# Performance work log

Measured on AMD Instinct MI355X. Metric: run time of the kernel, lower is better.

The kernel has to match this reference:

```python
import jax, jax.numpy as jnp
import numpy as np

EPS = 1e-5

def setup_inputs() -> dict:
    key = jax.random.key(0)
    k1, k2, k3, k4, k5 = jax.random.split(key, 5)
    B, D, S = 4096, 2048, 16384
    return {
        "x": jax.random.normal(k1, (B, D), dtype=jnp.float32),
        "W_enc": jax.random.normal(k2, (S, D), dtype=jnp.float32) * 0.02,  # encoder.weight [n_sae, n_input]
        "W_dec": jax.random.normal(k3, (D, S), dtype=jnp.float32) * 0.02,  # decoder.weight [n_input, n_sae]
        "pre_bias": jax.random.normal(k4, (D,), dtype=jnp.float32) * 0.01,
        "sae_bias": jax.random.normal(k5, (S,), dtype=jnp.float32) * 0.01,
        "k": 64,
    }

def reference(x, W_enc, W_dec, pre_bias, sae_bias, k):
    # --- pre_process: layer norm (torch.std is unbiased -> ddof=1) ---
    x_mean = jnp.mean(x, axis=-1, keepdims=True)
    std = jnp.std(x, axis=-1, ddof=1, keepdims=True)
    x_ln = (x - x_mean) / (std + EPS)
    # --- encode: latents_pre = (x_ln - pre_bias) @ W_enc^T + sae_bias ---
    pre_activations = (x_ln - pre_bias) @ W_enc.T + sae_bias  # [B, n_sae]
    # --- TopK activation: keep top-k, ReLU them, zero the rest ---
    vals, idx = jax.lax.top_k(pre_activations, k)              # [B, k]
    vals = jax.nn.relu(vals)
    rows = jnp.arange(pre_activations.shape[0])[:, None]       # [B, 1]
    latents = jnp.zeros_like(pre_activations).at[rows, idx].set(vals)
    # --- decode + un-normalize ---
    recons = latents @ W_dec.T + pre_bias                      # [B, n_input]
    recons = recons * std + x_mean
    return pre_activations, latents, recons
```

## Files before the change

kernel.cpp:

```cpp
#include <hip/hip_runtime.h>
#include <cstdint>
#include <cstddef>

#define EPSV 1e-5f
#define CAP 224
#define PAD 16
#define DELTA 0.02f
#define AMBCAP 64

__device__ __forceinline__ unsigned short f2bf(float f) {
  unsigned u = __float_as_uint(f);
  unsigned r = (u + 0x7FFFu + ((u >> 16) & 1u)) >> 16;
  return (unsigned short)r;
}
__device__ __forceinline__ float bf2f(unsigned short h) {
  return __uint_as_float(((unsigned)h) << 16);
}

__global__ __launch_bounds__(256) void ln_kernel(const float* __restrict__ x,
    const float* __restrict__ pre_bias, float* __restrict__ a,
    unsigned short* __restrict__ A2,
    float* __restrict__ stats, int D) {
  const int b = blockIdx.x;
  const int tid = threadIdx.x;
  const float4* x4 = reinterpret_cast<const float4*>(x + (size_t)b * D);
  const float4* pb4 = reinterpret_cast<const float4*>(pre_bias);
  float4* a4 = reinterpret_cast<float4*>(a + (size_t)b * D);
  float4 v0 = x4[tid], v1 = x4[tid + 256];
  float s = v0.x + v0.y + v0.z + v0.w + v1.x + v1.y + v1.z + v1.w;
  float ss = v0.x*v0.x + v0.y*v0.y + v0.z*v0.z + v0.w*v0.w
           + v1.x*v1.x + v1.y*v1.y + v1.z*v1.z + v1.w*v1.w;
#pragma unroll
  for (int off = 1; off < 64; off <<= 1) { s += __shfl_xor(s, off); ss += __shfl_xor(ss, off); }
  __shared__ float wsum[4], wssq[4], bmean, bstd;
  int wave = tid >> 6;
  if ((tid & 63) == 0) { wsum[wave] = s; wssq[wave] = ss; }
  __syncthreads();
  if (tid == 0) {
    float S1 = wsum[0] + wsum[1] + wsum[2] + wsum[3];
    float S2 = wssq[0] + wssq[1] + wssq[2] + wssq[3];
    float mean = S1 / (float)D;
    float var = (S2 - (float)D * mean * mean) / (float)(D - 1);
    float sd = sqrtf(fmaxf(var, 0.f));
    bmean = mean; bstd = sd;
    stats[2*b] = mean; stats[2*b+1] = sd;
  }
  __syncthreads();
  float mean = bmean, rstd = 1.f / (bstd + EPSV);
  float4 p0 = pb4[tid], p1 = pb4[tid + 256];
  float4 o0, o1;
  o0.x = (v0.x - mean) * rstd - p0.x; o0.y = (v0.y - mean) * rstd - p0.y;
  o0.z = (v0.z - mean) * rstd - p0.z; o0.w = (v0.w - mean) * rstd - p0.w;
  o1.x = (v1.x - mean) * rstd - p1.x; o1.y = (v1.y - mean) * rstd - p1.y;
  o1.z = (v1.z - mean) * rstd - p1.z; o1.w = (v1.w - mean) * rstd - p1.w;
  a4[tid] = o0; a4[tid + 256] = o1;
  if (A2) {
    unsigned short* row = A2 + (size_t)b * 2048;
    ushort4 h0 = make_ushort4(f2bf(o0.x), f2bf(o0.y), f2bf(o0.z), f2bf(o0.w));
    ushort4 h1 = make_ushort4(f2bf(o1.x), f2bf(o1.y), f2bf(o1.z), f2bf(o1.w));
    *reinterpret_cast<ushort4*>(row + tid * 4) = h0;
    *reinterpret_cast<ushort4*>(row + 1024 + tid * 4) = h1;
  }
}

__global__ __launch_bounds__(256) void cvt_w_kernel(const float* __restrict__ W,
    unsigned short* __restrict__ W2, int D) {
  const int s = blockIdx.x, tid = threadIdx.x;
  const float4* w4 = reinterpret_cast<const float4*>(W + (size_t)s * D);
  unsigned short* row = W2 + (size_t)s * D;
  float4 v0 = w4[tid * 2], v1 = w4[tid * 2 + 1];
  uint4 p;
  p.x = (unsigned)f2bf(v0.x) | ((unsigned)f2bf(v0.y) << 16);
  p.y = (unsigned)f2bf(v0.z) | ((unsigned)f2bf(v0.w) << 16);
  p.z = (unsigned)f2bf(v1.x) | ((unsigned)f2bf(v1.y) << 16);
  p.w = (unsigned)f2bf(v1.z) | ((unsigned)f2bf(v1.w) << 16);
  *reinterpret_cast<uint4*>(row + tid * 8) = p;
}

typedef __attribute__((ext_vector_type(8))) short bf8;
typedef __attribute__((ext_vector_type(4))) float f32x4;

__device__ __forceinline__ void gload16(const void* g, void* l) {
  __builtin_amdgcn_global_load_lds(
      (const __attribute__((address_space(1))) unsigned int*)g,
      (__attribute__((address_space(3))) unsigned int*)l,
      16, 0, 0);
}

__global__ __launch_bounds__(256) void enc_gemm_bf16(
    const unsigned short* __restrict__ A2,
    const unsigned short* __restrict__ W2,
    const float* __restrict__ sae_bias,
    float* __restrict__ C, int M, int N) {
  __shared__ __align__(16) short As0[128 * 64];
  __shared__ __align__(16) short Bs0[128 * 64];
  __shared__ __align__(16) short As1[128 * 64];
  __shared__ __align__(16) short Bs1[128 * 64];
  const int tid = threadIdx.x;
  const int bn = blockIdx.x, bm = blockIdx.y;
  const int w = tid >> 6, l = tid & 63;

  const int lrow = l >> 3;
  const int lcol = ((l & 7) ^ lrow) * 8;
  const unsigned short* gA[4];
  const unsigned short* gB[4];
#pragma unroll
  for (int i = 0; i < 4; ++i) {
    int chunk = w * 4 + i;
    int row = chunk * 8 + lrow;
    gA[i] = A2 + (size_t)(bm * 128 + row) * 2048 + lcol;
    gB[i] = W2 + (size_t)(bn * 128 + row) * 2048 + lcol;
  }
  const int ldsOff = (w * 4) * 512 + l * 8;

  const int wm = (w >> 1) * 64, wn = (w & 1) * 64;
  const int r15 = l & 15, b7 = l & 7, u = l >> 4;
  const int colks0 = ((u + 0) ^ b7) * 8;
  const int colks1 = ((u + 4) ^ b7) * 8;
  const int baseA = (wm + r15) * 64;
  const int baseB = (wn + r15) * 64;

  f32x4 acc[4][4];
#pragma unroll
  for (int mi = 0; mi < 4; ++mi)
#pragma unroll
    for (int ni = 0; ni < 4; ++ni) acc[mi][ni] = (f32x4){0.f, 0.f, 0.f, 0.f};

#define STAGE(Adst, Bdst, koff)                                   \
  {                                                               \
    _Pragma("unroll")                                             \
    for (int i = 0; i < 4; ++i) {                                 \
      gload16(gA[i] + (koff), &(Adst)[ldsOff + i * 512]);         \
      gload16(gB[i] + (koff), &(Bdst)[ldsOff + i * 512]);         \
    }                                                             \
  }

#define COMPUTE(Asrc, Bsrc)                                       \
  {                                                               \
    _Pragma("unroll")                                             \
    for (int ks = 0; ks < 2; ++ks) {                              \
      const int ck = ks ? colks1 : colks0;                        \
      bf8 af[4], bfv[4];                                          \
      _Pragma("unroll")                                           \
      for (int mi = 0; mi < 4; ++mi)                              \
        af[mi] = *reinterpret_cast<const bf8*>(&(Asrc)[baseA + mi * 1024 + ck]); \
      _Pragma("unroll")                                           \
      for (int ni = 0; ni < 4; ++ni)                              \
        bfv[ni] = *reinterpret_cast<const bf8*>(&(Bsrc)[baseB + ni * 1024 + ck]); \
      __builtin_amdgcn_s_setprio(1);                              \
      _Pragma("unroll")                                           \
      for (int mi = 0; mi < 4; ++mi)                              \
        _Pragma("unroll")                                         \
        for (int ni = 0; ni < 4; ++ni)                            \
          acc[mi][ni] = __builtin_amdgcn_mfma_f32_16x16x32_bf16(  \
              af[mi], bfv[ni], acc[mi][ni], 0, 0, 0);             \
      __builtin_amdgcn_s_setprio(0);                              \
    }                                                             \
  }

#define SYNC_TILE()                                               \
  {                                                               \
    asm volatile("s_waitcnt vmcnt(0)" ::: "memory");              \
    __builtin_amdgcn_s_barrier();                                 \
    asm volatile("" ::: "memory");                                \
  }

  STAGE(As0, Bs0, 0);
  SYNC_TILE();

  for (int t = 0; t < 32; t += 2) {
    STAGE(As1, Bs1, (t + 1) * 64);
    COMPUTE(As0, Bs0);
    SYNC_TILE();
    if (t + 2 < 32) STAGE(As0, Bs0, (t + 2) * 64);
    COMPUTE(As1, Bs1);
    SYNC_TILE();
  }
#undef STAGE
#undef COMPUTE
#undef SYNC_TILE

  const int cm = (l >> 4) * 4, cn = l & 15;
  float sb[4];
#pragma unroll
  for (int ni = 0; ni < 4; ++ni)
    sb[ni] = sae_bias[bn * 128 + wn + ni * 16 + cn];
#pragma unroll
  for (int mi = 0; mi < 4; ++mi) {
#pragma unroll
    for (int r = 0; r < 4; ++r) {
      int row = bm * 128 + wm + mi * 16 + cm + r;
      float* Crow = C + (size_t)row * N + bn * 128 + wn;
#pragma unroll
      for (int ni = 0; ni < 4; ++ni)
        Crow[ni * 16 + cn] = acc[mi][ni][r] + sb[ni];
    }
  }
}

#define BM 128
#define BN 128
#define BK 32
#define LDP 136

__global__ __launch_bounds__(256) void enc_gemm_f32(
    const float* __restrict__ A, const float* __restrict__ Bw,
    const float* __restrict__ sae_bias, float* __restrict__ C,
    int M, int N, int K) {
  __shared__ __align__(16) float As[BK * LDP];
  __shared__ __align__(16) float Bs[BK * LDP];
  const int tid = threadIdx.x;
  const int bn = blockIdx.x, bm = blockIdx.y;
  const float* Ab = A + (size_t)bm * BM * K;
  const float* Bb = Bw + (size_t)bn * BN * K;
  float acc[8][8];
#pragma unroll
  for (int i = 0; i < 8; ++i)
#pragma unroll
    for (int j = 0; j < 8; ++j) acc[i][j] = 0.f;
  const int tn = tid & 15, tm = tid >> 4;
  const int lk = tid & 31;
  const int lm4 = (tid >> 5) * 4;
  for (int k0 = 0; k0 < K; k0 += BK) {
#pragma unroll
    for (int i = 0; i < 4; ++i) {
      int mb = i * 32 + lm4;
      float a0 = Ab[(size_t)(mb + 0) * K + k0 + lk];
      float a1 = Ab[(size_t)(mb + 1) * K + k0 + lk];
      float a2 = Ab[(size_t)(mb + 2) * K + k0 + lk];
      float a3 = Ab[(size_t)(mb + 3) * K + k0 + lk];
      *reinterpret_cast<float4*>(&As[lk * LDP + mb]) = make_float4(a0, a1, a2, a3);
      float b0 = Bb[(size_t)(mb + 0) * K + k0 + lk];
      float b1 = Bb[(size_t)(mb + 1) * K + k0 + lk];
      float b2 = Bb[(size_t)(mb + 2) * K + k0 + lk];
      float b3 = Bb[(size_t)(mb + 3) * K + k0 + lk];
      *reinterpret_cast<float4*>(&Bs[lk * LDP + mb]) = make_float4(b0, b1, b2, b3);
    }
    __syncthreads();
#pragma unroll 8
    for (int kk = 0; kk < BK; ++kk) {
      float4 a0 = *reinterpret_cast<const float4*>(&As[kk * LDP + tm * 4]);
      float4 a1 = *reinterpret_cast<const float4*>(&As[kk * LDP + tm * 4 + 64]);
      float4 b0 = *reinterpret_cast<const float4*>(&Bs[kk * LDP + tn * 4]);
      float4 b1 = *reinterpret_cast<const float4*>(&Bs[kk * LDP + tn * 4 + 64]);
      float av[8] = {a0.x, a0.y, a0.z, a0.w, a1.x, a1.y, a1.z, a1.w};
      float bv[8] = {b0.x, b0.y, b0.z, b0.w, b1.x, b1.y, b1.z, b1.w};
#pragma unroll
      for (int ii = 0; ii < 8; ++ii)
#pragma unroll
        for (int jj = 0; jj < 8; ++jj)
          acc[ii][jj] = fmaf(av[ii], bv[jj], acc[ii][jj]);
    }
    __syncthreads();
  }
  float4 sb0 = *reinterpret_cast<const float4*>(sae_bias + bn * BN + tn * 4);
  float4 sb1 = *reinterpret_cast<const float4*>(sae_bias + bn * BN + tn * 4 + 64);
#pragma unroll
  for (int ii = 0; ii < 8; ++ii) {
    int row = bm * BM + (ii < 4 ? tm * 4 + ii : 64 + tm * 4 + ii - 4);
    float* Crow = C + (size_t)row * N + bn * BN;
    float4 o0 = make_float4(acc[ii][0] + sb0.x, acc[ii][1] + sb0.y,
                            acc[ii][2] + sb0.z, acc[ii][3] + sb0.w);
    float4 o1 = make_float4(acc[ii][4] + sb1.x, acc[ii][5] + sb1.y,
                            acc[ii][6] + sb1.z, acc[ii][7] + sb1.w);
    *reinterpret_cast<float4*>(Crow + tn * 4) = o0;
    *reinterpret_cast<float4*>(Crow + tn * 4 + 64) = o1;
  }
}

__device__ __forceinline__ unsigned mapf(float f) {
  unsigned u = __float_as_uint(f);
  return (u & 0x80000000u) ? ~u : (u | 0x80000000u);
}

__global__ __launch_bounds__(256) void topk_select(
    const float* __restrict__ preact, float* __restrict__ latents,
    const int* __restrict__ kp, int* __restrict__ cand, float* __restrict__ candv,
    int* __restrict__ candcnt, int S) {
  const int b = blockIdx.x, tid = threadIdx.x;
  const float4* row4 = reinterpret_cast<const float4*>(preact + (size_t)b * S);
  __shared__ int hist[4096];
  __shared__ int tsum[256];
  __shared__ unsigned sh_pref, sh_thr;
  __shared__ int sh_done, sh_cum, sh_cnt;
  int K = kp[0]; if (K > 192) K = 192;
  const int r = K + PAD;
  if (tid == 0) { sh_done = 0; sh_pref = 0; sh_cum = 0; }
  for (int level = 0; level < 3; ++level) {
    __syncthreads();
    if (sh_done) break;
    const int shift = (level == 0) ? 20 : (level == 1) ? 8 : 0;
    const int width = (level == 2) ? 8 : 12;
    const int nb = 1 << width;
    const unsigned mask = (unsigned)nb - 1;
    for (int i = tid; i < nb; i += 256) hist[i] = 0;
    __syncthreads();
    const unsigned pref = sh_pref;
    for (int i = tid; i < S / 4; i += 256) {
      float4 v = row4[i];
      unsigned uu[4] = {mapf(v.x), mapf(v.y), mapf(v.z), mapf(v.w)};
#pragma unroll
      for (int q = 0; q < 4; ++q) {
        bool ok = (level == 0) || ((uu[q] >> (shift + width)) == pref);
        if (ok) atomicAdd(&hist[(uu[q] >> shift) & mask], 1);
      }
    }
    __syncthreads();
    const int per = nb >> 8;
    int myts = 0;
#pragma unroll 4
    for (int j = 0; j < per; ++j) myts += hist[tid * per + j];
    tsum[tid] = myts;
    __syncthreads();
    for (int o = 1; o < 256; o <<= 1) {
      int v_ = (tid + o < 256) ? tsum[tid + o] : 0;
      __syncthreads();
      tsum[tid] += v_;
      __syncthreads();
    }
    const int rr = r - sh_cum;
    const int sufIncl = tsum[tid];
    const int sufExcl = sufIncl - myts;
    if (sufExcl < rr && rr <= sufIncl) {
      int running = sufExcl;
      for (int j = per - 1; j >= 0; --j) {
        int bb = tid * per + j;
        int c = hist[bb];
        if (running + c >= rr) {
          unsigned npref = (sh_pref << width) | (unsigned)bb;
          int candTotal = sh_cum + running + c;
          sh_pref = npref;
          sh_cum += running;
          if (candTotal <= CAP || level == 2) { sh_thr = npref << shift; sh_done = 1; }
          break;
        }
        running += c;
      }
    }
  }
  __syncthreads();
  const unsigned T = sh_thr;
  if (tid == 0) sh_cnt = 0;
  __syncthreads();
  float4* lat4 = reinterpret_cast<float4*>(latents + (size_t)b * S);
  float4 z = make_float4(0.f, 0.f, 0.f, 0.f);
  for (int i = tid; i < S / 4; i += 256) {
    float4 v = row4[i];
    unsigned uu[4] = {mapf(v.x), mapf(v.y), mapf(v.z), mapf(v.w)};
    float vv[4] = {v.x, v.y, v.z, v.w};
#pragma unroll
    for (int q = 0; q < 4; ++q) {
      if (uu[q] >= T) {
        int p = atomicAdd(&sh_cnt, 1);
        if (p < CAP) { cand[(size_t)b * CAP + p] = i * 4 + q; candv[(size_t)b * CAP + p] = vv[q]; }
      }
    }
    lat4[i] = z;
  }
  __syncthreads();
  if (tid == 0) candcnt[b] = (sh_cnt < CAP) ? sh_cnt : CAP;
}

__global__ __launch_bounds__(256) void topk_refine(
    const float* __restrict__ a, const float* __restrict__ W_enc,
    const float* __restrict__ sae_bias, const int* __restrict__ kp,
    const int* __restrict__ cand, const float* __restrict__ candv,
    const int* __restrict__ candcnt,
    float* __restrict__ latents, int* __restrict__ out_idx, float* __restrict__ out_val,
    int D, int S) {
  const int b = blockIdx.x, tid = threadIdx.x;
  __shared__ float sv[256];
  __shared__ int si[256];
  __shared__ double sv64[256];
  __shared__ double av[AMBCAP];
  __shared__ int aslot[AMBCAP], agid[AMBCAP];
  __shared__ int sh_amb, sh_nin;
  int K = kp[0]; if (K > 192) K = 192;
  const int cnt = candcnt[b];
  const int wave = tid >> 6, lane = tid & 63;
  const float4* ar4 = reinterpret_cast<const float4*>(a + (size_t)b * D);
  const int nit = D / 256;

  if (tid < cnt) { sv[tid] = candv[(size_t)b * CAP + tid]; si[tid] = cand[(size_t)b * CAP + tid]; }
  else { sv[tid] = -3.0e38f; si[tid] = 0x7FFFFFFF; }
  __syncthreads();
  for (int ksz = 2; ksz <= 256; ksz <<= 1) {
    for (int j = ksz >> 1; j > 0; j >>= 1) {
      int ixj = tid ^ j;
      if (ixj > tid) {
        float v1 = sv[tid], v2 = sv[ixj];
        int i1 = si[tid], i2 = si[ixj];
        bool dirDesc = ((tid & ksz) == 0);
        bool firstBetter = (v1 > v2) || (v1 == v2 && i1 < i2);
        if (dirDesc ? (!firstBetter) : firstBetter) {
          sv[tid] = v2; sv[ixj] = v1; si[tid] = i2; si[ixj] = i1;
        }
      }
      __syncthreads();
    }
  }
  const float vK = sv[K - 1];
  if (tid == 0) { sh_amb = 0; sh_nin = 0; }
  __syncthreads();
  bool isC = tid < cnt;
  if (isC && (sv[tid] > vK + DELTA)) atomicAdd(&sh_nin, 1);
  if (isC && fabsf(sv[tid] - vK) <= DELTA) {
    int p = atomicAdd(&sh_amb, 1);
    if (p < AMBCAP) { aslot[p] = tid; agid[p] = si[tid]; }
  }
  __syncthreads();
  const int nAmb = sh_amb, nIn = sh_nin;

  if (nAmb <= AMBCAP) {
    for (int c = wave; c < nAmb; c += 4) {
      int sidx = agid[c];
      const float4* wr4 = reinterpret_cast<const float4*>(W_enc + (size_t)sidx * D);
      double acc = 0.0;
      for (int m = 0; m < nit; ++m) {
        float4 a_ = ar4[m * 64 + lane];
        float4 w_ = wr4[m * 64 + lane];
        acc += (double)a_.x * w_.x + (double)a_.y * w_.y
             + (double)a_.z * w_.z + (double)a_.w * w_.w;
      }
#pragma unroll
      for (int off = 1; off < 64; off <<= 1) acc += __shfl_xor(acc, off);
      if (lane == 0) av[c] = acc + (double)sae_bias[sidx];
    }
    __syncthreads();
    if (tid < AMBCAP && tid >= nAmb) { av[tid] = -1.0e300; agid[tid] = 0x7FFFFFFF; }
    __syncthreads();
    for (int ksz = 2; ksz <= AMBCAP; ksz <<= 1) {
      for (int j = ksz >> 1; j > 0; j >>= 1) {
        int ixj = tid ^ j;
        if (tid < AMBCAP && ixj > tid) {
          double v1 = av[tid], v2 = av[ixj];
          int i1 = agid[tid], i2 = agid[ixj];
          bool dirDesc = ((tid & ksz) == 0);
          bool firstBetter = (v1 > v2) || (v1 == v2 && i1 < i2);
          if (dirDesc ? (!firstBetter) : firstBetter) {
            av[tid] = v2; av[ixj] = v1; agid[tid] = i2; agid[ixj] = i1;
          }
        }
        __syncthreads();
      }
    }
    if (tid < K) {
      int gidx; float val;
      if (tid < nIn) { gidx = si[tid]; val = sv[tid]; }
      else { int c = tid - nIn; gidx = agid[c]; val = (float)av[c]; }
      val = fmaxf(val, 0.f);
      latents[(size_t)b * S + gidx] = val;
      out_idx[(size_t)b * 256 + tid] = gidx;
      out_val[(size_t)b * 256 + tid] = val;
    }
  } else {
    for (int c = wave; c < cnt; c += 4) {
      int sidx = si[c];
      const float4* wr4 = reinterpret_cast<const float4*>(W_enc + (size_t)sidx * D);
      double acc = 0.0;
      for (int m = 0; m < nit; ++m) {
        float4 a_ = ar4[m * 64 + lane];
        float4 w_ = wr4[m * 64 + lane];
        acc += (double)a_.x * w_.x + (double)a_.y * w_.y
             + (double)a_.z * w_.z + (double)a_.w * w_.w;
      }
#pragma unroll
      for (int off = 1; off < 64; off <<= 1) acc += __shfl_xor(acc, off);
      if (lane == 0) sv64[c] = acc + (double)sae_bias[sidx];
    }
    __syncthreads();
    if (tid >= cnt) { sv64[tid] = -1.0e300; si[tid] = 0x7FFFFFFF; }
    __syncthreads();
    for (int ksz = 2; ksz <= 256; ksz <<= 1) {
      for (int j = ksz >> 1; j > 0; j >>= 1) {
        int ixj = tid ^ j;
        if (ixj > tid) {
          double v1 = sv64[tid], v2 = sv64[ixj];
          int i1 = si[tid], i2 = si[ixj];
          bool dirDesc = ((tid & ksz) == 0);
          bool firstBetter = (v1 > v2) || (v1 == v2 && i1 < i2);
          if (dirDesc ? (!firstBetter) : firstBetter) {
            sv64[tid] = v2; sv64[ixj] = v1; si[tid] = i2; si[ixj] = i1;
          }
        }
        __syncthreads();
      }
    }
    if (tid < K) {
      int idx = si[tid];
      float rv = fmaxf((float)sv64[tid], 0.f);
      latents[(size_t)b * S + idx] = rv;
      out_idx[(size_t)b * 256 + tid] = idx;
      out_val[(size_t)b * 256 + tid] = rv;
    }
  }
}

__global__ __launch_bounds__(256) void transpose_cvt(const float* __restrict__ src,
    unsigned short* __restrict__ dst, int D, int S) {
  __shared__ float t[32][33];
  int s0 = blockIdx.x * 32, d0 = blockIdx.y * 32;
  int tx = threadIdx.x & 31, ty = threadIdx.x >> 5;
#pragma unroll
  for (int i = 0; i < 32; i += 8)
    t[ty + i][tx] = src[(size_t)(d0 + ty + i) * S + s0 + tx];
  __syncthreads();
#pragma unroll
  for (int i = 0; i < 32; i += 8)
    dst[(size_t)(s0 + ty + i) * D + d0 + tx] = f2bf(t[tx][ty + i]);
}

__global__ __launch_bounds__(256) void decode_bf16(
    const unsigned short* __restrict__ WdTh, const float* __restrict__ pre_bias,
    const float* __restrict__ stats, const int* __restrict__ kp,
    const int* __restrict__ out_idx, const float* __restrict__ out_val,
    float* __restrict__ recons, int D) {
  const int b = blockIdx.x, tid = threadIdx.x;
  __shared__ int sidx[192];
  __shared__ float sval[192];
  int K = kp[0]; if (K > 192) K = 192;
  if (tid < K) { sidx[tid] = out_idx[(size_t)b * 256 + tid]; sval[tid] = out_val[(size_t)b * 256 + tid]; }
  __syncthreads();
  const int c0 = tid * 8;
  float4 p0 = *reinterpret_cast<const float4*>(pre_bias + c0);
  float4 p1 = *reinterpret_cast<const float4*>(pre_bias + c0 + 4);
  float acc[8] = {p0.x, p0.y, p0.z, p0.w, p1.x, p1.y, p1.z, p1.w};
  for (int j = 0; j < K; ++j) {
    float v = sval[j];
    uint4 wv = *reinterpret_cast<const uint4*>(WdTh + (size_t)sidx[j] * D + c0);
    acc[0] = fmaf(v, bf2f((unsigned short)(wv.x & 0xffff)), acc[0]);
    acc[1] = fmaf(v, bf2f((unsigned short)(wv.x >> 16)),    acc[1]);
    acc[2] = fmaf(v, bf2f((unsigned short)(wv.y & 0xffff)), acc[2]);
    acc[3] = fmaf(v, bf2f((unsigned short)(wv.y >> 16)),    acc[3]);
    acc[4] = fmaf(v, bf2f((unsigned short)(wv.z & 0xffff)), acc[4]);
    acc[5] = fmaf(v, bf2f((unsigned short)(wv.z >> 16)),    acc[5]);
    acc[6] = fmaf(v, bf2f((unsigned short)(wv.w & 0xffff)), acc[6]);
    acc[7] = fmaf(v, bf2f((unsigned short)(wv.w >> 16)),    acc[7]);
  }
  float mean = stats[2 * b], sd = stats[2 * b + 1];
  float4 o0 = make_float4(acc[0] * sd + mean, acc[1] * sd + mean,
                          acc[2] * sd + mean, acc[3] * sd + mean);
  float4 o1 = make_float4(acc[4] * sd + mean, acc[5] * sd + mean,
                          acc[6] * sd + mean, acc[7] * sd + mean);
  float* r = recons + (size_t)b * D + c0;
  *reinterpret_cast<float4*>(r) = o0;
  *reinterpret_cast<float4*>(r + 4) = o1;
}

__global__ __launch_bounds__(256) void decode_fb(
    const float* __restrict__ Wd, const float* __restrict__ pre_bias,
    const float* __restrict__ stats, const int* __restrict__ kp,
    const int* __restrict__ out_idx, const float* __restrict__ out_val,
    float* __restrict__ recons, int D, int S) {
  const int b = blockIdx.x, tid = threadIdx.x;
  __shared__ int sidx[192];
  __shared__ float sval[192];
  int K = kp[0]; if (K > 192) K = 192;
  if (tid < K) { sidx[tid] = out_idx[(size_t)b * 256 + tid]; sval[tid] = out_val[(size_t)b * 256 + tid]; }
  __syncthreads();
  for (int d = tid; d < D; d += 256) {
    float acc = pre_bias[d];
    for (int j = 0; j < K; ++j)
      acc = fmaf(sval[j], Wd[(size_t)d * S + sidx[j]], acc);
    recons[(size_t)b * D + d] = acc * stats[2 * b + 1] + stats[2 * b];
  }
}

extern "C" void kernel_launch(void* const* d_in, const int* in_sizes, int n_in,
                              void* d_out, int out_size, void* d_ws, size_t ws_size,
                              hipStream_t stream) {
  const float* x        = (const float*)d_in[0];
  const float* W_enc    = (const float*)d_in[1];
  const float* W_dec    = (const float*)d_in[2];
  const float* pre_bias = (const float*)d_in[3];
  const float* sae_bias = (const float*)d_in[4];
  const int*   kp       = (const int*)d_in[5];
  const int D = in_sizes[3];
  const int S = in_sizes[4];
  const int B = in_sizes[0] / D;

  float* out_pre = (float*)d_out;
  float* out_lat = out_pre + (size_t)B * S;
  float* out_rec = out_lat + (size_t)B * S;

  char* ws = (char*)d_ws;
  size_t off = 0;
  float* a = (float*)(ws + off);        off += (size_t)B * D * 4;
  float* stats = (float*)(ws + off);    off += (size_t)B * 2 * 4;
  int* cand = (int*)(ws + off);         off += (size_t)B * CAP * 4;
  float* candv = (float*)(ws + off);    off += (size_t)B * CAP * 4;
  int* candcnt = (int*)(ws + off);      off += (size_t)B * 4;
  int* oidx = (int*)(ws + off);         off += (size_t)B * 256 * 4;
  float* oval = (float*)(ws + off);     off += (size_t)B * 256 * 4;
  off = (off + 255) & ~(size_t)255;
  unsigned short* A2 = (unsigned short*)(ws + off);
  size_t offW2 = off + (size_t)B * D * 2;
  unsigned short* W2 = (unsigned short*)(ws + offW2);
  size_t offWdT = offW2 + (size_t)S * D * 2;
  unsigned short* WdTh = (unsigned short*)(ws + offWdT);
  size_t offEnd = offWdT + (size_t)S * D * 2;
  bool useBf16 = (D == 2048) && (B % 128 == 0) && (S % 128 == 0) &&
                 (S % 32 == 0) && (D % 32 == 0) && (ws_size >= offEnd);

  if (useBf16) {
    ln_kernel<<<B, 256, 0, stream>>>(x, pre_bias, a, A2, stats, D);
    cvt_w_kernel<<<S, 256, 0, stream>>>(W_enc, W2, D);
    enc_gemm_bf16<<<dim3(S / 128, B / 128), 256, 0, stream>>>(A2, W2, sae_bias, out_pre, B, S);
    transpose_cvt<<<dim3(S / 32, D / 32), 256, 0, stream>>>(W_dec, WdTh, D, S);
    topk_select<<<B, 256, 0, stream>>>(out_pre, out_lat, kp, cand, candv, candcnt, S);
    topk_refine<<<B, 256, 0, stream>>>(a, W_enc, sae_bias, kp, cand, candv, candcnt,
                                       out_lat, oidx, oval, D, S);
    decode_bf16<<<B, 256, 0, stream>>>(WdTh, pre_bias, stats, kp, oidx, oval, out_rec, D);
  } else {
    ln_kernel<<<B, 256, 0, stream>>>(x, pre_bias, a, nullptr, stats, D);
    enc_gemm_f32<<<dim3(S / BN, B / BM), 256, 0, stream>>>(a, W_enc, sae_bias, out_pre, B, S, D);
    topk_select<<<B, 256, 0, stream>>>(out_pre, out_lat, kp, cand, candv, candcnt, S);
    topk_refine<<<B, 256, 0, stream>>>(a, W_enc, sae_bias, kp, cand, candv, candcnt,
                                       out_lat, oidx, oval, D, S);
    decode_fb<<<B, 256, 0, stream>>>(W_dec, pre_bias, stats, kp, oidx, oval, out_rec, D, S);
  }
}
```

Baseline: 862.2 us.

## Use 512-thread blocks for bf16 encoder GEMM and decoder, widen top-k ambiguity band

The bf16 encoder GEMM now runs 8 waves per 128x128 tile, each computing a 64x32 sub-tile, with reworked global-to-LDS load mapping. The decoder uses 512 threads, each handling 4 output columns instead of 8. The top-k refine ambiguity band DELTA is widened and an unused shared array is removed. The aim is more waves to hide latency and fewer registers per thread, at the cost of lower MFMA reuse per wave and more fp64 refinement work in top-k.

```diff
diff --git a/kernel.cpp b/kernel.cpp
--- a/kernel.cpp
+++ b/kernel.cpp
@@ -5,7 +5,7 @@
 #define EPSV 1e-5f
 #define CAP 224
 #define PAD 16
-#define DELTA 0.02f
+#define DELTA 0.03f
 #define AMBCAP 64
 
 __device__ __forceinline__ unsigned short f2bf(float f) {
@@ -87,7 +87,7 @@
       16, 0, 0);
 }
 
-__global__ __launch_bounds__(256) void enc_gemm_bf16(
+__global__ __launch_bounds__(512) void enc_gemm_bf16(
     const unsigned short* __restrict__ A2,
     const unsigned short* __restrict__ W2,
     const float* __restrict__ sae_bias,
@@ -100,38 +100,38 @@
   const int bn = blockIdx.x, bm = blockIdx.y;
   const int w = tid >> 6, l = tid & 63;
 
-  const int lrow = l >> 3;
-  const int lcol = ((l & 7) ^ lrow) * 8;
-  const unsigned short* gA[4];
-  const unsigned short* gB[4];
-#pragma unroll
-  for (int i = 0; i < 4; ++i) {
-    int chunk = w * 4 + i;
-    int row = chunk * 8 + lrow;
-    gA[i] = A2 + (size_t)(bm * 128 + row) * 2048 + lcol;
-    gB[i] = W2 + (size_t)(bn * 128 + row) * 2048 + lcol;
-  }
-  const int ldsOff = (w * 4) * 512 + l * 8;
-
-  const int wm = (w >> 1) * 64, wn = (w & 1) * 64;
+  const unsigned short* gA[2];
+  const unsigned short* gB[2];
+  int ldsSlot[2];
+#pragma unroll
+  for (int r = 0; r < 2; ++r) {
+    int slot = r * 512 + tid;
+    int row = slot >> 3, unit = slot & 7;
+    int gcol = (unit ^ (row & 7)) * 8;
+    gA[r] = A2 + (size_t)(bm * 128 + row) * 2048 + gcol;
+    gB[r] = W2 + (size_t)(bn * 128 + row) * 2048 + gcol;
+    ldsSlot[r] = slot * 8;
+  }
+
+  const int wm = (w >> 2) * 64, wn = (w & 3) * 32;
   const int r15 = l & 15, b7 = l & 7, u = l >> 4;
   const int colks0 = ((u + 0) ^ b7) * 8;
   const int colks1 = ((u + 4) ^ b7) * 8;
   const int baseA = (wm + r15) * 64;
   const int baseB = (wn + r15) * 64;
 
-  f32x4 acc[4][4];
+  f32x4 acc[4][2];
 #pragma unroll
   for (int mi = 0; mi < 4; ++mi)
 #pragma unroll
-    for (int ni = 0; ni < 4; ++ni) acc[mi][ni] = (f32x4){0.f, 0.f, 0.f, 0.f};
+    for (int ni = 0; ni < 2; ++ni) acc[mi][ni] = (f32x4){0.f, 0.f, 0.f, 0.f};
 
 #define STAGE(Adst, Bdst, koff)                                   \
   {                                                               \
     _Pragma("unroll")                                             \
-    for (int i = 0; i < 4; ++i) {                                 \
-      gload16(gA[i] + (koff), &(Adst)[ldsOff + i * 512]);         \
-      gload16(gB[i] + (koff), &(Bdst)[ldsOff + i * 512]);         \
+    for (int r = 0; r < 2; ++r) {                                 \
+      gload16(gA[r] + (koff), &(Adst)[ldsSlot[r]]);               \
+      gload16(gB[r] + (koff), &(Bdst)[ldsSlot[r]]);               \
     }                                                             \
   }
 
@@ -140,18 +140,18 @@
     _Pragma("unroll")                                             \
     for (int ks = 0; ks < 2; ++ks) {                              \
       const int ck = ks ? colks1 : colks0;                        \
-      bf8 af[4], bfv[4];                                          \
+      bf8 af[4], bfv[2];                                          \
       _Pragma("unroll")                                           \
       for (int mi = 0; mi < 4; ++mi)                              \
         af[mi] = *reinterpret_cast<const bf8*>(&(Asrc)[baseA + mi * 1024 + ck]); \
       _Pragma("unroll")                                           \
-      for (int ni = 0; ni < 4; ++ni)                              \
+      for (int ni = 0; ni < 2; ++ni)                              \
         bfv[ni] = *reinterpret_cast<const bf8*>(&(Bsrc)[baseB + ni * 1024 + ck]); \
       __builtin_amdgcn_s_setprio(1);                              \
       _Pragma("unroll")                                           \
       for (int mi = 0; mi < 4; ++mi)                              \
         _Pragma("unroll")                                         \
-        for (int ni = 0; ni < 4; ++ni)                            \
+        for (int ni = 0; ni < 2; ++ni)                            \
           acc[mi][ni] = __builtin_amdgcn_mfma_f32_16x16x32_bf16(  \
               af[mi], bfv[ni], acc[mi][ni], 0, 0, 0);             \
       __builtin_amdgcn_s_setprio(0);                              \
@@ -181,9 +181,9 @@
 #undef SYNC_TILE
 
   const int cm = (l >> 4) * 4, cn = l & 15;
-  float sb[4];
-#pragma unroll
-  for (int ni = 0; ni < 4; ++ni)
+  float sb[2];
+#pragma unroll
+  for (int ni = 0; ni < 2; ++ni)
     sb[ni] = sae_bias[bn * 128 + wn + ni * 16 + cn];
 #pragma unroll
   for (int mi = 0; mi < 4; ++mi) {
@@ -192,7 +192,7 @@
       int row = bm * 128 + wm + mi * 16 + cm + r;
       float* Crow = C + (size_t)row * N + bn * 128 + wn;
 #pragma unroll
-      for (int ni = 0; ni < 4; ++ni)
+      for (int ni = 0; ni < 2; ++ni)
         Crow[ni * 16 + cn] = acc[mi][ni][r] + sb[ni];
     }
   }
@@ -373,7 +373,7 @@
   __shared__ int si[256];
   __shared__ double sv64[256];
   __shared__ double av[AMBCAP];
-  __shared__ int aslot[AMBCAP], agid[AMBCAP];
+  __shared__ int agid[AMBCAP];
   __shared__ int sh_amb, sh_nin;
   int K = kp[0]; if (K > 192) K = 192;
   const int cnt = candcnt[b];
@@ -406,7 +406,7 @@
   if (isC && (sv[tid] > vK + DELTA)) atomicAdd(&sh_nin, 1);
   if (isC && fabsf(sv[tid] - vK) <= DELTA) {
     int p = atomicAdd(&sh_amb, 1);
-    if (p < AMBCAP) { aslot[p] = tid; agid[p] = si[tid]; }
+    if (p < AMBCAP) agid[p] = si[tid];
   }
   __syncthreads();
   const int nAmb = sh_amb, nIn = sh_nin;
@@ -510,7 +510,7 @@
     dst[(size_t)(s0 + ty + i) * D + d0 + tx] = f2bf(t[tx][ty + i]);
 }
 
-__global__ __launch_bounds__(256) void decode_bf16(
+__global__ __launch_bounds__(512) void decode_bf16(
     const unsigned short* __restrict__ WdTh, const float* __restrict__ pre_bias,
     const float* __restrict__ stats, const int* __restrict__ kp,
     const int* __restrict__ out_idx, const float* __restrict__ out_val,
@@ -521,30 +521,21 @@
   int K = kp[0]; if (K > 192) K = 192;
   if (tid < K) { sidx[tid] = out_idx[(size_t)b * 256 + tid]; sval[tid] = out_val[(size_t)b * 256 + tid]; }
   __syncthreads();
-  const int c0 = tid * 8;
+  const int c0 = tid * 4;
   float4 p0 = *reinterpret_cast<const float4*>(pre_bias + c0);
-  float4 p1 = *reinterpret_cast<const float4*>(pre_bias + c0 + 4);
-  float acc[8] = {p0.x, p0.y, p0.z, p0.w, p1.x, p1.y, p1.z, p1.w};
+  float acc0 = p0.x, acc1 = p0.y, acc2 = p0.z, acc3 = p0.w;
   for (int j = 0; j < K; ++j) {
     float v = sval[j];
-    uint4 wv = *reinterpret_cast<const uint4*>(WdTh + (size_t)sidx[j] * D + c0);
-    acc[0] = fmaf(v, bf2f((unsigned short)(wv.x & 0xffff)), acc[0]);
-    acc[1] = fmaf(v, bf2f((unsigned short)(wv.x >> 16)),    acc[1]);
-    acc[2] = fmaf(v, bf2f((unsigned short)(wv.y & 0xffff)), acc[2]);
-    acc[3] = fmaf(v, bf2f((unsigned short)(wv.y >> 16)),    acc[3]);
-    acc[4] = fmaf(v, bf2f((unsigned short)(wv.z & 0xffff)), acc[4]);
-    acc[5] = fmaf(v, bf2f((unsigned short)(wv.z >> 16)),    acc[5]);
-    acc[6] = fmaf(v, bf2f((unsigned short)(wv.w & 0xffff)), acc[6]);
-    acc[7] = fmaf(v, bf2f((unsigned short)(wv.w >> 16)),    acc[7]);
+    uint2 wv = *reinterpret_cast<const uint2*>(WdTh + (size_t)sidx[j] * D + c0);
+    acc0 = fmaf(v, bf2f((unsigned short)(wv.x & 0xffff)), acc0);
+    acc1 = fmaf(v, bf2f((unsigned short)(wv.x >> 16)),    acc1);
+    acc2 = fmaf(v, bf2f((unsigned short)(wv.y & 0xffff)), acc2);
+    acc3 = fmaf(v, bf2f((unsigned short)(wv.y >> 16)),    acc3);
   }
   float mean = stats[2 * b], sd = stats[2 * b + 1];
-  float4 o0 = make_float4(acc[0] * sd + mean, acc[1] * sd + mean,
-                          acc[2] * sd + mean, acc[3] * sd + mean);
-  float4 o1 = make_float4(acc[4] * sd + mean, acc[5] * sd + mean,
-                          acc[6] * sd + mean, acc[7] * sd + mean);
-  float* r = recons + (size_t)b * D + c0;
-  *reinterpret_cast<float4*>(r) = o0;
-  *reinterpret_cast<float4*>(r + 4) = o1;
+  float4 o = make_float4(acc0 * sd + mean, acc1 * sd + mean,
+                         acc2 * sd + mean, acc3 * sd + mean);
+  *reinterpret_cast<float4*>(recons + (size_t)b * D + c0) = o;
 }
 
 __global__ __launch_bounds__(256) void decode_fb(
@@ -605,12 +596,12 @@
   if (useBf16) {
     ln_kernel<<<B, 256, 0, stream>>>(x, pre_bias, a, A2, stats, D);
     cvt_w_kernel<<<S, 256, 0, stream>>>(W_enc, W2, D);
-    enc_gemm_bf16<<<dim3(S / 128, B / 128), 256, 0, stream>>>(A2, W2, sae_bias, out_pre, B, S);
+    enc_gemm_bf16<<<dim3(S / 128, B / 128), 512, 0, stream>>>(A2, W2, sae_bias, out_pre, B, S);
     transpose_cvt<<<dim3(S / 32, D / 32), 256, 0, stream>>>(W_dec, WdTh, D, S);
     topk_select<<<B, 256, 0, stream>>>(out_pre, out_lat, kp, cand, candv, candcnt, S);
     topk_refine<<<B, 256, 0, stream>>>(a, W_enc, sae_bias, kp, cand, candv, candcnt,
                                        out_lat, oidx, oval, D, S);
-    decode_bf16<<<B, 256, 0, stream>>>(WdTh, pre_bias, stats, kp, oidx, oval, out_rec, D);
+    decode_bf16<<<B, 512, 0, stream>>>(WdTh, pre_bias, stats, kp, oidx, oval, out_rec, D);
   } else {
     ln_kernel<<<B, 256, 0, stream>>>(x, pre_bias, a, nullptr, stats, D);
     enc_gemm_f32<<<dim3(S / BN, B / BM), 256, 0, stream>>>(a, W_enc, sae_bias, out_pre, B, S, D);
```

New measurement: 850.7 us. Within noise of the previous version (-1.3%).
